# Kernel optimization log

Measured on AMD Instinct MI355X. Metric: run time of the kernel, lower is better.

The kernel has to match this reference:

```python
import jax, jax.numpy as jnp
import numpy as np
import math

B, S, D, H, F = 2, 2048, 1024, 16, 4096
DK = D // H
NEG_INF = -1000000000.0
EPS = 1e-5


def _layernorm(x, gamma, beta):
    # Faithful to source: torch.std default is unbiased (ddof=1), eps added to std
    mn = jnp.mean(x, axis=-1, keepdims=True)
    sd = jnp.std(x, axis=-1, keepdims=True, ddof=1)
    return (x - mn) / (sd + EPS) * gamma + beta


def _mha(xq, xkv, wq, bq, wk, bk, wv, bv, wo, bo, causal):
    b, sq, d = xq.shape
    sk = xkv.shape[1]
    q = (xq @ wq + bq).reshape(b, sq, H, DK).transpose(0, 2, 1, 3)   # [B,H,Sq,DK]
    k = (xkv @ wk + bk).reshape(b, sk, H, DK).transpose(0, 2, 1, 3)
    v = (xkv @ wv + bv).reshape(b, sk, H, DK).transpose(0, 2, 1, 3)
    scores = jnp.einsum('bhqd,bhkd->bhqk', q, k) / math.sqrt(DK)
    if causal:
        mask = jnp.triu(jnp.ones((sq, sk), dtype=scores.dtype), 1) * NEG_INF
        scores = scores + mask
    w = jax.nn.softmax(scores, axis=-1)
    att = jnp.einsum('bhqk,bhkd->bhqd', w, v).transpose(0, 2, 1, 3).reshape(b, sq, d)
    return att @ wo + bo


def setup_inputs() -> dict:
    key = jax.random.key(0)
    ks = jax.random.split(key, 32)
    it = iter(range(32))

    def lin(din, dout):
        kw = ks[next(it)]
        w = jax.random.normal(kw, (din, dout), jnp.float32) / math.sqrt(din)
        b = jnp.zeros((dout,), jnp.float32)
        return w, b

    X = jax.random.normal(ks[next(it)], (B, S, D), jnp.float32)
    y = jax.random.normal(ks[next(it)], (B, S, D), jnp.float32)
    wq1, bq1 = lin(D, D); wk1, bk1 = lin(D, D); wv1, bv1 = lin(D, D); wo1, bo1 = lin(D, D)
    wq2, bq2 = lin(D, D); wk2, bk2 = lin(D, D); wv2, bv2 = lin(D, D); wo2, bo2 = lin(D, D)
    wf1, bf1 = lin(D, F); wf2, bf2 = lin(F, D)
    g1 = jnp.ones((D,), jnp.float32); be1 = jnp.zeros((D,), jnp.float32)
    g2 = jnp.ones((D,), jnp.float32); be2 = jnp.zeros((D,), jnp.float32)
    g3 = jnp.ones((D,), jnp.float32); be3 = jnp.zeros((D,), jnp.float32)
    return dict(X=X, y=y,
                wq1=wq1, bq1=bq1, wk1=wk1, bk1=bk1, wv1=wv1, bv1=bv1, wo1=wo1, bo1=bo1,
                wq2=wq2, bq2=bq2, wk2=wk2, bk2=bk2, wv2=wv2, bv2=bv2, wo2=wo2, bo2=bo2,
                wf1=wf1, bf1=bf1, wf2=wf2, bf2=bf2,
                g1=g1, be1=be1, g2=g2, be2=be2, g3=g3, be3=be3)


def reference(X, y,
              wq1, bq1, wk1, bk1, wv1, bv1, wo1, bo1,
              wq2, bq2, wk2, bk2, wv2, bv2, wo2, bo2,
              wf1, bf1, wf2, bf2,
              g1, be1, g2, be2, g3, be3):
    # masked self-attention on decoder stream y (dropout = identity at inference)
    res = y
    out = _mha(y, y, wq1, bq1, wk1, bk1, wv1, bv1, wo1, bo1, causal=True)
    out = _layernorm(out + res, g1, be1)
    # cross-attention: queries from decoder, keys/values from encoder X
    res = out
    out = _mha(out, X, wq2, bq2, wk2, bk2, wv2, bv2, wo2, bo2, causal=False)
    out = _layernorm(out + res, g2, be2)
    # feed-forward (ReLU per intended semantics of the source)
    res = out
    out = jax.nn.relu(out @ wf1 + bf1) @ wf2 + bf2
    out = _layernorm(out + res, g3, be3)
    return out
```

## Files before the change

kernel.cpp:

```cpp
#include <hip/hip_runtime.h>

#define DEV __device__ __forceinline__

typedef __attribute__((ext_vector_type(8))) short short8;
typedef __attribute__((ext_vector_type(4))) float f32x4;
typedef __attribute__((ext_vector_type(4))) unsigned u32x4;

DEV unsigned short f2b(float f){
  unsigned r;
  asm("v_cvt_pk_bf16_f32 %0, %1, %1" : "=v"(r) : "v"(f));
  return (unsigned short)r;
}
DEV unsigned cvt_pk2(float lo, float hi){
  unsigned r;
  asm("v_cvt_pk_bf16_f32 %0, %1, %2" : "=v"(r) : "v"(lo), "v"(hi));
  return r;
}
DEV float b2f(unsigned short u){ unsigned v = ((unsigned)u)<<16; float f; __builtin_memcpy(&f,&v,4); return f; }

DEV void gload_lds16(const void* g, void* l){
  __builtin_amdgcn_global_load_lds((const __attribute__((address_space(1))) void*)g,
                                   (__attribute__((address_space(3))) void*)l, 16, 0, 0);
}

#define SCL 0.18033688011112042f

__global__ __launch_bounds__(256) void cvt_f32_bf16(
    const float* __restrict__ in, unsigned short* __restrict__ out, int n)
{
  int i = (blockIdx.x*256 + threadIdx.x)*4;
  if (i >= n) return;
  float4 v = *(const float4*)(in + i);
  uint2 o;
  o.x = cvt_pk2(v.x, v.y);
  o.y = cvt_pk2(v.z, v.w);
  *(uint2*)(out + i) = o;
}

struct TransAll {
  const float* W[10]; unsigned short* Wt[10];
  int K[10], N[10], swapxy[10];
};
__global__ __launch_bounds__(256) void transpose_cvt_all(TransAll p)
{
  const int z = blockIdx.z;
  const int bx = p.swapxy[z] ? blockIdx.y : blockIdx.x;
  const int by = p.swapxy[z] ? blockIdx.x : blockIdx.y;
  const int K = p.K[z], N = p.N[z];
  const int n0 = bx*32, k0 = by*32;
  if (n0 >= N || k0 >= K) return;
  const float* __restrict__ W = p.W[z];
  unsigned short* __restrict__ Wt = p.Wt[z];
  __shared__ float tile[32][33];
  int tx = threadIdx.x & 31, ty = threadIdx.x >> 5;
  #pragma unroll
  for (int j=0;j<32;j+=8)
    tile[ty+j][tx] = W[(size_t)(k0+ty+j)*N + n0+tx];
  __syncthreads();
  #pragma unroll
  for (int j=0;j<32;j+=8)
    Wt[(size_t)(n0+ty+j)*K + k0+tx] = f2b(tile[tx][ty+j]);
}

template<int EPI>
__global__ __launch_bounds__(256) void gemm_bt(
    const unsigned short* __restrict__ A,
    const unsigned short* __restrict__ Bt,
    const float* __restrict__ bias,
    unsigned short* __restrict__ C,
    int M, int N, int Kc, int LDA, int LDB)
{
  __shared__ alignas(16) unsigned short Asm_[128*64];
  __shared__ alignas(16) unsigned short Bsm_[128*64];
  const int tid = threadIdx.x;
  const int wave = tid>>6, lane = tid&63;
  const int r0 = lane&15, kq = (lane>>4)*8, cq = lane>>4;
  const int m0 = blockIdx.y*128, n0 = blockIdx.x*128;
  const int wr = wave>>1, wc = wave&1;
  const int koff = blockIdx.z * Kc;
  const bool addb = (blockIdx.z == 0);
  C += (size_t)blockIdx.z * M * N;
  const int swr = (r0&7)<<3;

  f32x4 zero4 = {0.f,0.f,0.f,0.f};
  f32x4 acc[4][4];
  #pragma unroll
  for (int m=0;m<4;m++)
    #pragma unroll
    for (int n=0;n<4;n++) acc[m][n]=zero4;

  const int nk = Kc>>6;
  for (int kt=0; kt<nk; kt++){
    #pragma unroll
    for (int i=0;i<4;i++){
      int idx = i*256 + tid;
      int row = idx>>3;
      int sc = ((idx&7) ^ (row&7))<<3;
      gload_lds16(A  + (size_t)(m0+row)*LDA + koff + (kt<<6) + sc, Asm_ + (size_t)idx*8);
      gload_lds16(Bt + (size_t)(n0+row)*LDB + koff + (kt<<6) + sc, Bsm_ + (size_t)idx*8);
    }
    __syncthreads();
    #pragma unroll
    for (int kk=0;kk<2;kk++){
      short8 a[4], b[4];
      #pragma unroll
      for (int m=0;m<4;m++)
        a[m] = *(const short8*)&Asm_[(((wr*64 + m*16 + r0)*64) + kk*32 + kq) ^ swr];
      #pragma unroll
      for (int n=0;n<4;n++)
        b[n] = *(const short8*)&Bsm_[(((wc*64 + n*16 + r0)*64) + kk*32 + kq) ^ swr];
      #pragma unroll
      for (int m=0;m<4;m++)
        #pragma unroll
        for (int n=0;n<4;n++)
          acc[m][n] = __builtin_amdgcn_mfma_f32_16x16x32_bf16(a[m], b[n], acc[m][n], 0,0,0);
    }
    __syncthreads();
  }

  #pragma unroll
  for (int n=0;n<4;n++){
    int col = n0 + wc*64 + n*16 + r0;
    float bs = addb ? bias[col] : 0.f;
    #pragma unroll
    for (int m=0;m<4;m++){
      int rowb = m0 + wr*64 + m*16 + cq*4;
      #pragma unroll
      for (int reg=0;reg<4;reg++){
        float v = acc[m][n][reg] + bs;
        if (EPI==1) v = fmaxf(v, 0.f);
        C[(size_t)(rowb+reg)*N + col] = f2b(v);
      }
    }
  }
}

struct QKVArgs { const unsigned short* Aw[3]; const float* bias[3]; unsigned short* out[3]; };
__global__ __launch_bounds__(256) void gemm_qkv(
    const unsigned short* __restrict__ Bt,
    QKVArgs args, int M, int K)
{
  __shared__ alignas(16) unsigned short Asm_[128*64];
  __shared__ alignas(16) unsigned short Bsm_[128*64];
  const int tid = threadIdx.x;
  const int wave = tid>>6, lane = tid&63;
  const int r0 = lane&15, kq = (lane>>4)*8, cq = lane>>4;
  const int m0 = blockIdx.y*128, n0 = blockIdx.x*128;
  const int wr = wave>>1, wc = wave&1;
  const int which = n0>>10;
  const unsigned short* __restrict__ A = args.Aw[which];
  const int swr = (r0&7)<<3;

  f32x4 zero4 = {0.f,0.f,0.f,0.f};
  f32x4 acc[4][4];
  #pragma unroll
  for (int m=0;m<4;m++)
    #pragma unroll
    for (int n=0;n<4;n++) acc[m][n]=zero4;

  const int nk = K>>6;
  for (int kt=0; kt<nk; kt++){
    #pragma unroll
    for (int i=0;i<4;i++){
      int idx = i*256 + tid;
      int row = idx>>3;
      int sc = ((idx&7) ^ (row&7))<<3;
      gload_lds16(A  + (size_t)(m0+row)*K + (kt<<6) + sc, Asm_ + (size_t)idx*8);
      gload_lds16(Bt + (size_t)(n0+row)*K + (kt<<6) + sc, Bsm_ + (size_t)idx*8);
    }
    __syncthreads();
    #pragma unroll
    for (int kk=0;kk<2;kk++){
      short8 a[4], b[4];
      #pragma unroll
      for (int m=0;m<4;m++)
        a[m] = *(const short8*)&Asm_[(((wr*64 + m*16 + r0)*64) + kk*32 + kq) ^ swr];
      #pragma unroll
      for (int n=0;n<4;n++)
        b[n] = *(const short8*)&Bsm_[(((wc*64 + n*16 + r0)*64) + kk*32 + kq) ^ swr];
      #pragma unroll
      for (int m=0;m<4;m++)
        #pragma unroll
        for (int n=0;n<4;n++)
          acc[m][n] = __builtin_amdgcn_mfma_f32_16x16x32_bf16(a[m], b[n], acc[m][n], 0,0,0);
    }
    __syncthreads();
  }

  const int n0l = n0 & 1023;
  unsigned short* __restrict__ Cout = args.out[which];
  const float* __restrict__ bp = args.bias[which];
  const bool isV = (which == 2);
  const float scl = (which == 0) ? SCL : 1.f;

  #pragma unroll
  for (int n=0;n<4;n++){
    int col = n0l + wc*64 + n*16 + r0;
    float bs = bp[col];
    int h_ = col>>6, dk = col&63;
    #pragma unroll
    for (int m=0;m<4;m++){
      int rowb = m0 + wr*64 + m*16 + cq*4;
      #pragma unroll
      for (int reg=0;reg<4;reg++){
        float v = (acc[m][n][reg] + bs) * scl;
        int row = rowb + reg;
        int b_ = row>>11, s_ = row&2047;
        if (isV){
          int sp = (s_ & ~31) | (((s_>>2)&3)<<3) | (((s_>>4)&1)<<2) | (s_&3);
          Cout[(((size_t)(b_*16+h_))*64 + dk)*2048 + sp] = f2b(v);
        } else {
          Cout[(((size_t)(b_*16+h_))*2048 + s_)*64 + dk] = f2b(v);
        }
      }
    }
  }
}

template<int MODE>
__global__ __launch_bounds__(256, 4) void attn_kernel(
    const unsigned short* __restrict__ Q,
    const unsigned short* __restrict__ K,
    const unsigned short* __restrict__ Vt,
    unsigned short* __restrict__ O,
    float* __restrict__ po, unsigned short* __restrict__ pob,
    float* __restrict__ ml)
{
  __shared__ alignas(16) unsigned short Ksm[2][64*64];
  __shared__ alignas(16) unsigned short Vsm[2][64*64];
  const int S = 2048, DK = 64;
  const int h = blockIdx.y, b = blockIdx.z;
  const int tid = threadIdx.x, wave = tid>>6, lane = tid&63;
  const int r0 = lane&15, kq = (lane>>4)*8, cq = lane>>4;

  int qb, t0, t1, chunk = 0;
  bool partial = false;
  if (MODE==1){
    int bx = blockIdx.x;
    if (bx < 32){ qb = bx; t0 = 0; t1 = (qb<15?qb:15); chunk = 0; partial = (qb>=16); }
    else        { qb = bx-16; t0 = 16; t1 = qb; chunk = 1; partial = true; }
  } else {
    int bx = blockIdx.x;
    if (bx < 32){ qb = bx; t0 = 0; t1 = 15; chunk = 0; }
    else        { qb = bx-32; t0 = 16; t1 = 31; chunk = 1; }
    partial = true;
  }

  const unsigned short* qh = Q  + ((size_t)(b*16+h))*S*DK;
  const unsigned short* kh = K  + ((size_t)(b*16+h))*S*DK;
  const unsigned short* vh = Vt + ((size_t)(b*16+h))*DK*S;

  const int idx0 = tid, idx1 = 256 + tid;
  const int row0 = idx0>>3, row1 = idx1>>3;
  const int cb0 = ((idx0&7) ^ (row0&7))<<3;
  const int cb1 = ((idx1&7) ^ (row1&7))<<3;
  const unsigned short* kg0 = kh + (size_t)row0*64 + cb0;
  const unsigned short* kg1 = kh + (size_t)row1*64 + cb1;
  const unsigned short* vg0 = vh + (size_t)row0*2048 + cb0;
  const unsigned short* vg1 = vh + (size_t)row1*2048 + cb1;
  const int l0 = wave*512, l1 = 2048 + wave*512;
  const int swr = (r0&7)<<3;

  short8 qa[2];
  {
    int qrow = qb*64 + wave*16 + r0;
    qa[0] = *(const short8*)&qh[(size_t)qrow*DK + kq];
    qa[1] = *(const short8*)&qh[(size_t)qrow*DK + 32 + kq];
  }
  short8 vones;
  #pragma unroll
  for (int j=0;j<8;j++) vones[j] = (short)0x3F80;

  f32x4 zero4 = {0.f,0.f,0.f,0.f};
  f32x4 o[4];
  float lr = 0.f;
  #pragma unroll
  for (int n=0;n<4;n++) o[n]=zero4;

  gload_lds16(kg0 + (size_t)t0*4096, &Ksm[0][l0]);
  gload_lds16(kg1 + (size_t)t0*4096, &Ksm[0][l1]);
  gload_lds16(vg0 + (size_t)t0*64,   &Vsm[0][l0]);
  gload_lds16(vg1 + (size_t)t0*64,   &Vsm[0][l1]);

  int cur = 0;
  for (int t=t0; t<=t1; t++){
    if (t < t1){
      gload_lds16(kg0 + (size_t)(t+1)*4096, &Ksm[cur^1][l0]);
      gload_lds16(kg1 + (size_t)(t+1)*4096, &Ksm[cur^1][l1]);
      gload_lds16(vg0 + (size_t)(t+1)*64,   &Vsm[cur^1][l0]);
      gload_lds16(vg1 + (size_t)(t+1)*64,   &Vsm[cur^1][l1]);
      asm volatile("s_waitcnt vmcnt(4)" ::: "memory");
    } else {
      asm volatile("s_waitcnt vmcnt(0)" ::: "memory");
    }
    __builtin_amdgcn_s_barrier();
    asm volatile("" ::: "memory");

    f32x4 sv[4];
    #pragma unroll
    for (int n=0;n<4;n++) sv[n]=zero4;
    #pragma unroll
    for (int n=0;n<4;n++)
      #pragma unroll
      for (int kk=0;kk<2;kk++){
        short8 kb = *(const short8*)&Ksm[cur][(((n*16 + r0)*64) + kk*32 + kq) ^ swr];
        sv[n] = __builtin_amdgcn_mfma_f32_16x16x32_bf16(kb, qa[kk], sv[n], 0,0,0);
      }
    if (MODE==1 && t==qb){
      const int qg = wave*16 + r0;
      #pragma unroll
      for (int n=0;n<4;n++)
        #pragma unroll
        for (int reg=0;reg<4;reg++){
          if (n*16 + cq*4 + reg > qg) sv[n][reg] += -1000000000.0f;
        }
    }

    #pragma unroll
    for (int n=0;n<4;n++)
      #pragma unroll
      for (int reg=0;reg<4;reg++)
        sv[n][reg] = exp2f(sv[n][reg]);

    short8 pa[2];
    #pragma unroll
    for (int kk=0;kk<2;kk++){
      u32x4 w;
      w[0] = cvt_pk2(sv[2*kk][0],   sv[2*kk][1]);
      w[1] = cvt_pk2(sv[2*kk][2],   sv[2*kk][3]);
      w[2] = cvt_pk2(sv[2*kk+1][0], sv[2*kk+1][1]);
      w[3] = cvt_pk2(sv[2*kk+1][2], sv[2*kk+1][3]);
      pa[kk] = __builtin_bit_cast(short8, w);
    }

    {
      f32x4 ls = zero4;
      ls = __builtin_amdgcn_mfma_f32_16x16x32_bf16(vones, pa[0], ls, 0,0,0);
      ls = __builtin_amdgcn_mfma_f32_16x16x32_bf16(vones, pa[1], ls, 0,0,0);
      lr += ls[0];
    }

    #pragma unroll
    for (int n=0;n<4;n++)
      #pragma unroll
      for (int kk=0;kk<2;kk++){
        short8 vb = *(const short8*)&Vsm[cur][(((n*16 + r0)*64) + kk*32 + cq*8) ^ swr];
        o[n] = __builtin_amdgcn_mfma_f32_16x16x32_bf16(vb, pa[kk], o[n], 0,0,0);
      }

    asm volatile("" ::: "memory");
    __builtin_amdgcn_s_barrier();
    asm volatile("" ::: "memory");
    cur ^= 1;
  }

  if (MODE==1 && partial){
    float* pop = po + (size_t)chunk*2097152;
    float* mlp = ml + (size_t)chunk*32768;
    const int bh = b*16 + h, qb16 = qb - 16;
    const int rowIdx = (bh*16 + qb16)*64 + wave*16 + r0;
    if (cq == 0) mlp[rowIdx] = lr;
    #pragma unroll
    for (int n=0;n<4;n++){
      float4 v; v.x=o[n][0]; v.y=o[n][1]; v.z=o[n][2]; v.w=o[n][3];
      *(float4*)&pop[(size_t)rowIdx*64 + n*16 + cq*4] = v;
    }
  } else if (MODE==2){
    unsigned short* pop = pob + (size_t)chunk*4194304;
    float* mlp = ml + (size_t)chunk*65536;
    const int bh = b*16 + h;
    const int rowIdx = (bh*32 + qb)*64 + wave*16 + r0;
    if (cq == 0) mlp[rowIdx] = lr;
    #pragma unroll
    for (int n=0;n<4;n++){
      uint2 w;
      w.x = cvt_pk2(o[n][0], o[n][1]);
      w.y = cvt_pk2(o[n][2], o[n][3]);
      *(uint2*)(pop + (size_t)rowIdx*64 + n*16 + cq*4) = w;
    }
  } else {
    const int sg = qb*64 + wave*16 + r0;
    const float inv = 1.f / lr;
    unsigned short* op = O + ((size_t)b*S + sg)*1024 + h*64;
    #pragma unroll
    for (int n=0;n<4;n++){
      uint2 w;
      w.x = cvt_pk2(o[n][0]*inv, o[n][1]*inv);
      w.y = cvt_pk2(o[n][2]*inv, o[n][3]*inv);
      *(uint2*)(op + n*16 + cq*4) = w;
    }
  }
}

__global__ __launch_bounds__(256) void attn_merge(
    const float* __restrict__ po, const float* __restrict__ ml,
    unsigned short* __restrict__ O)
{
  int gid = blockIdx.x*256 + threadIdx.x;
  int row = gid>>4, dq = (gid&15)*4;
  float l0 = ml[row], l1 = ml[32768 + row];
  float inv = 1.f / (l0 + l1);
  float4 v0 = *(const float4*)(po + (size_t)row*64 + dq);
  float4 v1 = *(const float4*)(po + 2097152 + (size_t)row*64 + dq);
  float r0 = (v0.x + v1.x)*inv;
  float r1 = (v0.y + v1.y)*inv;
  float r2 = (v0.z + v1.z)*inv;
  float r3 = (v0.w + v1.w)*inv;
  int bh = row>>10, qb16 = (row>>6)&15, qr = row&63;
  int b = bh>>4, h = bh&15;
  int s = (16+qb16)*64 + qr;
  unsigned short* op = O + ((size_t)b*2048 + s)*1024 + h*64 + dq;
  uint2 out; out.x = cvt_pk2(r0, r1); out.y = cvt_pk2(r2, r3);
  *(uint2*)op = out;
}

__global__ __launch_bounds__(256) void attn_merge_x(
    const unsigned short* __restrict__ pob, const float* __restrict__ ml,
    unsigned short* __restrict__ O)
{
  int gid = blockIdx.x*256 + threadIdx.x;
  int row = gid>>4, dq = (gid&15)*4;
  float l0 = ml[row], l1 = ml[65536 + row];
  float inv = 1.f / (l0 + l1);
  ushort4 u0 = *(const ushort4*)(pob + (size_t)row*64 + dq);
  ushort4 u1 = *(const ushort4*)(pob + 4194304 + (size_t)row*64 + dq);
  float r0 = (b2f(u0.x) + b2f(u1.x))*inv;
  float r1 = (b2f(u0.y) + b2f(u1.y))*inv;
  float r2 = (b2f(u0.z) + b2f(u1.z))*inv;
  float r3 = (b2f(u0.w) + b2f(u1.w))*inv;
  int bh = row>>11, s = row&2047;
  int b = bh>>4, h = bh&15;
  unsigned short* op = O + ((size_t)b*2048 + s)*1024 + h*64 + dq;
  uint2 out; out.x = cvt_pk2(r0, r1); out.y = cvt_pk2(r2, r3);
  *(uint2*)op = out;
}

template<int OUT_F32>
__global__ __launch_bounds__(256) void add_ln3(
    const unsigned short* __restrict__ a0, const unsigned short* __restrict__ a1,
    const unsigned short* __restrict__ r,
    const float* __restrict__ g, const float* __restrict__ be, void* outp)
{
  const int row = blockIdx.x, tid = threadIdx.x;
  const size_t base = (size_t)row*1024 + tid*4;
  ushort4 va = *(const ushort4*)(a0 + base);
  ushort4 vb_ = *(const ushort4*)(a1 + base);
  ushort4 vr = *(const ushort4*)(r + base);
  float x[4];
  x[0] = b2f(va.x)+b2f(vb_.x)+b2f(vr.x);
  x[1] = b2f(va.y)+b2f(vb_.y)+b2f(vr.y);
  x[2] = b2f(va.z)+b2f(vb_.z)+b2f(vr.z);
  x[3] = b2f(va.w)+b2f(vb_.w)+b2f(vr.w);
  float s = x[0]+x[1]+x[2]+x[3];
  float ss = x[0]*x[0]+x[1]*x[1]+x[2]*x[2]+x[3]*x[3];
  #pragma unroll
  for (int d=1;d<64;d<<=1){ s += __shfl_xor(s,d,64); ss += __shfl_xor(ss,d,64); }
  __shared__ float rs[4], rss[4];
  int wave = tid>>6, lane = tid&63;
  if (lane==0){ rs[wave]=s; rss[wave]=ss; }
  __syncthreads();
  s = rs[0]+rs[1]+rs[2]+rs[3];
  ss = rss[0]+rss[1]+rss[2]+rss[3];
  float mean = s*(1.f/1024.f);
  float var = (ss - 1024.f*mean*mean)*(1.f/1023.f);
  float sd = sqrtf(fmaxf(var,0.f));
  float inv = 1.f/(sd + 1e-5f);
  float4 vg = *(const float4*)(g + tid*4);
  float4 vbe = *(const float4*)(be + tid*4);
  float o0 = (x[0]-mean)*inv*vg.x+vbe.x;
  float o1 = (x[1]-mean)*inv*vg.y+vbe.y;
  float o2 = (x[2]-mean)*inv*vg.z+vbe.z;
  float o3 = (x[3]-mean)*inv*vg.w+vbe.w;
  if (OUT_F32){
    float4 vo; vo.x=o0; vo.y=o1; vo.z=o2; vo.w=o3;
    *(float4*)((float*)outp + base) = vo;
  } else {
    uint2 vo; vo.x = cvt_pk2(o0,o1); vo.y = cvt_pk2(o2,o3);
    *(uint2*)((unsigned short*)outp + base) = vo;
  }
}

extern "C" void kernel_launch(void* const* d_in, const int* in_sizes, int n_in,
                              void* d_out, int out_size, void* d_ws, size_t ws_size,
                              hipStream_t stream)
{
  typedef const float* cf;
  cf X   = (cf)d_in[0],  y   = (cf)d_in[1];
  cf wq1 = (cf)d_in[2],  bq1 = (cf)d_in[3],  wk1 = (cf)d_in[4],  bk1 = (cf)d_in[5];
  cf wv1 = (cf)d_in[6],  bv1 = (cf)d_in[7],  wo1 = (cf)d_in[8],  bo1 = (cf)d_in[9];
  cf wq2 = (cf)d_in[10], bq2 = (cf)d_in[11], wk2 = (cf)d_in[12], bk2 = (cf)d_in[13];
  cf wv2 = (cf)d_in[14], bv2 = (cf)d_in[15], wo2 = (cf)d_in[16], bo2 = (cf)d_in[17];
  cf wf1 = (cf)d_in[18], bf1 = (cf)d_in[19], wf2 = (cf)d_in[20], bf2 = (cf)d_in[21];
  cf g1  = (cf)d_in[22], be1 = (cf)d_in[23], g2  = (cf)d_in[24], be2 = (cf)d_in[25];
  cf g3  = (cf)d_in[26], be3 = (cf)d_in[27];

  char* ws = (char*)d_ws;
  const size_t MB = 1u<<20;
  unsigned short* wq1t = (unsigned short*)(ws + 0*MB);
  unsigned short* wk1t = (unsigned short*)(ws + 2*MB);
  unsigned short* wv1t = (unsigned short*)(ws + 4*MB);
  unsigned short* wo1t = (unsigned short*)(ws + 6*MB);
  unsigned short* wq2t = (unsigned short*)(ws + 8*MB);
  unsigned short* wk2t = (unsigned short*)(ws + 10*MB);
  unsigned short* wv2t = (unsigned short*)(ws + 12*MB);
  unsigned short* wo2t = (unsigned short*)(ws + 14*MB);
  unsigned short* wf1t = (unsigned short*)(ws + 16*MB);
  unsigned short* wf2t = (unsigned short*)(ws + 24*MB);
  unsigned short* Qb   = (unsigned short*)(ws + 32*MB);
  unsigned short* Kb   = (unsigned short*)(ws + 40*MB);
  unsigned short* Vtb  = (unsigned short*)(ws + 48*MB);
  unsigned short* attno= (unsigned short*)(ws + 56*MB);
  unsigned short* hbuf = (unsigned short*)(ws + 32*MB);
  unsigned short* part = (unsigned short*)(ws + 64*MB);
  float*          poF  = (float*)(ws + 64*MB);
  unsigned short* pobF = (unsigned short*)(ws + 64*MB);
  float*          mlF  = (float*)(ws + 80*MB);
  unsigned short* x1b  = (unsigned short*)(ws + 80*MB);
  unsigned short* slot = (unsigned short*)(ws + 88*MB);
  unsigned short* yb = slot, *Xb = slot, *x2b = slot;
  float*          mlX  = (float*)(ws + 88*MB);

  dim3 blk(256);
  const int NTOK = 2*2048*1024;
  cvt_f32_bf16<<<NTOK/1024, blk, 0, stream>>>(y, yb, NTOK);

  {
    TransAll tp;
    const float* Ws[10]   = {wq1,wk1,wv1,wo1,wq2,wk2,wv2,wo2,wf1,wf2};
    unsigned short* Ts[10]= {wq1t,wk1t,wv1t,wo1t,wq2t,wk2t,wv2t,wo2t,wf1t,wf2t};
    for (int i=0;i<10;i++){
      tp.W[i]=Ws[i]; tp.Wt[i]=Ts[i];
      tp.K[i] = (i==9)?4096:1024;
      tp.N[i] = (i==8)?4096:1024;
      tp.swapxy[i] = (i==9)?1:0;
    }
    transpose_cvt_all<<<dim3(128,32,10), blk, 0, stream>>>(tp);
  }

  dim3 gqkv(24,32);
  dim3 gs(8,32,2);
  dim3 gff1(32,32,1);
  dim3 gac(48,16,2);
  dim3 gax(64,16,2);

  {
    QKVArgs a1;
    a1.Aw[0]=yb; a1.Aw[1]=yb; a1.Aw[2]=yb;
    a1.bias[0]=bq1; a1.bias[1]=bk1; a1.bias[2]=bv1;
    a1.out[0]=Qb; a1.out[1]=Kb; a1.out[2]=Vtb;
    gemm_qkv<<<gqkv, blk, 0, stream>>>(wq1t, a1, 4096, 1024);
  }
  attn_kernel<1><<<gac, blk, 0, stream>>>(Qb, Kb, Vtb, attno, poF, nullptr, mlF);
  attn_merge<<<2048, blk, 0, stream>>>(poF, mlF, attno);
  gemm_bt<0><<<gs, blk, 0, stream>>>(attno, wo1t, bo1, part, 4096, 1024, 512, 1024, 1024);
  add_ln3<0><<<4096, blk, 0, stream>>>(part, part+4194304, yb, g1, be1, x1b);

  cvt_f32_bf16<<<NTOK/1024, blk, 0, stream>>>(X, Xb, NTOK);
  {
    QKVArgs a2;
    a2.Aw[0]=x1b; a2.Aw[1]=Xb; a2.Aw[2]=Xb;
    a2.bias[0]=bq2; a2.bias[1]=bk2; a2.bias[2]=bv2;
    a2.out[0]=Qb; a2.out[1]=Kb; a2.out[2]=Vtb;
    gemm_qkv<<<gqkv, blk, 0, stream>>>(wq2t, a2, 4096, 1024);
  }
  attn_kernel<2><<<gax, blk, 0, stream>>>(Qb, Kb, Vtb, attno, nullptr, pobF, mlX);
  attn_merge_x<<<4096, blk, 0, stream>>>(pobF, mlX, attno);
  gemm_bt<0><<<gs, blk, 0, stream>>>(attno, wo2t, bo2, part, 4096, 1024, 512, 1024, 1024);
  add_ln3<0><<<4096, blk, 0, stream>>>(part, part+4194304, x1b, g2, be2, x2b);

  gemm_bt<1><<<gff1, blk, 0, stream>>>(x2b, wf1t, bf1, hbuf, 4096, 4096, 1024, 1024, 1024);
  gemm_bt<0><<<gs, blk, 0, stream>>>(hbuf, wf2t, bf2, part, 4096, 1024, 2048, 4096, 4096);
  add_ln3<1><<<4096, blk, 0, stream>>>(part, part+4194304, x2b, g3, be3, d_out);
}
```

Baseline: 385.4 us.

## Process two query tiles per block in cross-attention to reuse K/V tiles

Splits the templated attention kernel into a causal kernel and a dedicated cross-attention kernel. Each cross-attention block now handles 128 query rows, two 64-row sub-tiles per wave, against the same LDS-staged K/V tiles, so K/V global loads and barriers are shared across twice the queries. The grid is halved to match, and launch bounds drop to 2 blocks per CU because register use roughly doubles. The trade-off is lower occupancy and fewer blocks to hide latency, in exchange for less K/V traffic per query row.

```diff
diff --git a/kernel.cpp b/kernel.cpp
--- a/kernel.cpp
+++ b/kernel.cpp
@@ -217,14 +217,12 @@
   }
 }
 
-template<int MODE>
-__global__ __launch_bounds__(256, 4) void attn_kernel(
+__global__ __launch_bounds__(256, 4) void attn_causal(
     const unsigned short* __restrict__ Q,
     const unsigned short* __restrict__ K,
     const unsigned short* __restrict__ Vt,
     unsigned short* __restrict__ O,
-    float* __restrict__ po, unsigned short* __restrict__ pob,
-    float* __restrict__ ml)
+    float* __restrict__ po, float* __restrict__ ml)
 {
   __shared__ alignas(16) unsigned short Ksm[2][64*64];
   __shared__ alignas(16) unsigned short Vsm[2][64*64];
@@ -235,15 +233,10 @@
 
   int qb, t0, t1, chunk = 0;
   bool partial = false;
-  if (MODE==1){
+  {
     int bx = blockIdx.x;
     if (bx < 32){ qb = bx; t0 = 0; t1 = (qb<15?qb:15); chunk = 0; partial = (qb>=16); }
     else        { qb = bx-16; t0 = 16; t1 = qb; chunk = 1; partial = true; }
-  } else {
-    int bx = blockIdx.x;
-    if (bx < 32){ qb = bx; t0 = 0; t1 = 15; chunk = 0; }
-    else        { qb = bx-32; t0 = 16; t1 = 31; chunk = 1; }
-    partial = true;
   }
 
   const unsigned short* qh = Q  + ((size_t)(b*16+h))*S*DK;
@@ -258,7 +251,7 @@
   const unsigned short* kg1 = kh + (size_t)row1*64 + cb1;
   const unsigned short* vg0 = vh + (size_t)row0*2048 + cb0;
   const unsigned short* vg1 = vh + (size_t)row1*2048 + cb1;
-  const int l0 = wave*512, l1 = 2048 + wave*512;
+  const int ld0 = wave*512, ld1 = 2048 + wave*512;
   const int swr = (r0&7)<<3;
 
   short8 qa[2];
@@ -277,18 +270,18 @@
   #pragma unroll
   for (int n=0;n<4;n++) o[n]=zero4;
 
-  gload_lds16(kg0 + (size_t)t0*4096, &Ksm[0][l0]);
-  gload_lds16(kg1 + (size_t)t0*4096, &Ksm[0][l1]);
-  gload_lds16(vg0 + (size_t)t0*64,   &Vsm[0][l0]);
-  gload_lds16(vg1 + (size_t)t0*64,   &Vsm[0][l1]);
+  gload_lds16(kg0 + (size_t)t0*4096, &Ksm[0][ld0]);
+  gload_lds16(kg1 + (size_t)t0*4096, &Ksm[0][ld1]);
+  gload_lds16(vg0 + (size_t)t0*64,   &Vsm[0][ld0]);
+  gload_lds16(vg1 + (size_t)t0*64,   &Vsm[0][ld1]);
 
   int cur = 0;
   for (int t=t0; t<=t1; t++){
     if (t < t1){
-      gload_lds16(kg0 + (size_t)(t+1)*4096, &Ksm[cur^1][l0]);
-      gload_lds16(kg1 + (size_t)(t+1)*4096, &Ksm[cur^1][l1]);
-      gload_lds16(vg0 + (size_t)(t+1)*64,   &Vsm[cur^1][l0]);
-      gload_lds16(vg1 + (size_t)(t+1)*64,   &Vsm[cur^1][l1]);
+      gload_lds16(kg0 + (size_t)(t+1)*4096, &Ksm[cur^1][ld0]);
+      gload_lds16(kg1 + (size_t)(t+1)*4096, &Ksm[cur^1][ld1]);
+      gload_lds16(vg0 + (size_t)(t+1)*64,   &Vsm[cur^1][ld0]);
+      gload_lds16(vg1 + (size_t)(t+1)*64,   &Vsm[cur^1][ld1]);
       asm volatile("s_waitcnt vmcnt(4)" ::: "memory");
     } else {
       asm volatile("s_waitcnt vmcnt(0)" ::: "memory");
@@ -306,7 +299,7 @@
         short8 kb = *(const short8*)&Ksm[cur][(((n*16 + r0)*64) + kk*32 + kq) ^ swr];
         sv[n] = __builtin_amdgcn_mfma_f32_16x16x32_bf16(kb, qa[kk], sv[n], 0,0,0);
       }
-    if (MODE==1 && t==qb){
+    if (t==qb){
       const int qg = wave*16 + r0;
       #pragma unroll
       for (int n=0;n<4;n++)
@@ -354,7 +347,7 @@
     cur ^= 1;
   }
 
-  if (MODE==1 && partial){
+  if (partial){
     float* pop = po + (size_t)chunk*2097152;
     float* mlp = ml + (size_t)chunk*32768;
     const int bh = b*16 + h, qb16 = qb - 16;
@@ -365,19 +358,6 @@
       float4 v; v.x=o[n][0]; v.y=o[n][1]; v.z=o[n][2]; v.w=o[n][3];
       *(float4*)&pop[(size_t)rowIdx*64 + n*16 + cq*4] = v;
     }
-  } else if (MODE==2){
-    unsigned short* pop = pob + (size_t)chunk*4194304;
-    float* mlp = ml + (size_t)chunk*65536;
-    const int bh = b*16 + h;
-    const int rowIdx = (bh*32 + qb)*64 + wave*16 + r0;
-    if (cq == 0) mlp[rowIdx] = lr;
-    #pragma unroll
-    for (int n=0;n<4;n++){
-      uint2 w;
-      w.x = cvt_pk2(o[n][0], o[n][1]);
-      w.y = cvt_pk2(o[n][2], o[n][3]);
-      *(uint2*)(pop + (size_t)rowIdx*64 + n*16 + cq*4) = w;
-    }
   } else {
     const int sg = qb*64 + wave*16 + r0;
     const float inv = 1.f / lr;
@@ -389,6 +369,160 @@
       w.y = cvt_pk2(o[n][2]*inv, o[n][3]*inv);
       *(uint2*)(op + n*16 + cq*4) = w;
     }
+  }
+}
+
+__global__ __launch_bounds__(256, 2) void attn_cross2(
+    const unsigned short* __restrict__ Q,
+    const unsigned short* __restrict__ K,
+    const unsigned short* __restrict__ Vt,
+    unsigned short* __restrict__ pob,
+    float* __restrict__ ml)
+{
+  __shared__ alignas(16) unsigned short Ksm[2][64*64];
+  __shared__ alignas(16) unsigned short Vsm[2][64*64];
+  const int S = 2048, DK = 64;
+  const int h = blockIdx.y, b = blockIdx.z;
+  const int tid = threadIdx.x, wave = tid>>6, lane = tid&63;
+  const int r0 = lane&15, kq = (lane>>4)*8, cq = lane>>4;
+
+  int qB, t0, t1, chunk;
+  {
+    int bx = blockIdx.x;
+    if (bx < 16){ qB = bx; t0 = 0; t1 = 15; chunk = 0; }
+    else        { qB = bx-16; t0 = 16; t1 = 31; chunk = 1; }
+  }
+
+  const unsigned short* qh = Q  + ((size_t)(b*16+h))*S*DK;
+  const unsigned short* kh = K  + ((size_t)(b*16+h))*S*DK;
+  const unsigned short* vh = Vt + ((size_t)(b*16+h))*DK*S;
+
+  const int idx0 = tid, idx1 = 256 + tid;
+  const int row0 = idx0>>3, row1 = idx1>>3;
+  const int cb0 = ((idx0&7) ^ (row0&7))<<3;
+  const int cb1 = ((idx1&7) ^ (row1&7))<<3;
+  const unsigned short* kg0 = kh + (size_t)row0*64 + cb0;
+  const unsigned short* kg1 = kh + (size_t)row1*64 + cb1;
+  const unsigned short* vg0 = vh + (size_t)row0*2048 + cb0;
+  const unsigned short* vg1 = vh + (size_t)row1*2048 + cb1;
+  const int ld0 = wave*512, ld1 = 2048 + wave*512;
+  const int swr = (r0&7)<<3;
+
+  short8 qa0[2], qa1[2];
+  {
+    int qrow = qB*128 + wave*16 + r0;
+    qa0[0] = *(const short8*)&qh[(size_t)qrow*DK + kq];
+    qa0[1] = *(const short8*)&qh[(size_t)qrow*DK + 32 + kq];
+    qa1[0] = *(const short8*)&qh[(size_t)(qrow+64)*DK + kq];
+    qa1[1] = *(const short8*)&qh[(size_t)(qrow+64)*DK + 32 + kq];
+  }
+  short8 vones;
+  #pragma unroll
+  for (int j=0;j<8;j++) vones[j] = (short)0x3F80;
+
+  f32x4 zero4 = {0.f,0.f,0.f,0.f};
+  f32x4 o0[4], o1[4];
+  float lr0 = 0.f, lr1 = 0.f;
+  #pragma unroll
+  for (int n=0;n<4;n++){ o0[n]=zero4; o1[n]=zero4; }
+
+  gload_lds16(kg0 + (size_t)t0*4096, &Ksm[0][ld0]);
+  gload_lds16(kg1 + (size_t)t0*4096, &Ksm[0][ld1]);
+  gload_lds16(vg0 + (size_t)t0*64,   &Vsm[0][ld0]);
+  gload_lds16(vg1 + (size_t)t0*64,   &Vsm[0][ld1]);
+
+  int cur = 0;
+  for (int t=t0; t<=t1; t++){
+    if (t < t1){
+      gload_lds16(kg0 + (size_t)(t+1)*4096, &Ksm[cur^1][ld0]);
+      gload_lds16(kg1 + (size_t)(t+1)*4096, &Ksm[cur^1][ld1]);
+      gload_lds16(vg0 + (size_t)(t+1)*64,   &Vsm[cur^1][ld0]);
+      gload_lds16(vg1 + (size_t)(t+1)*64,   &Vsm[cur^1][ld1]);
+      asm volatile("s_waitcnt vmcnt(4)" ::: "memory");
+    } else {
+      asm volatile("s_waitcnt vmcnt(0)" ::: "memory");
+    }
+    __builtin_amdgcn_s_barrier();
+    asm volatile("" ::: "memory");
+
+    f32x4 sa[4], sb[4];
+    #pragma unroll
+    for (int n=0;n<4;n++){ sa[n]=zero4; sb[n]=zero4; }
+    #pragma unroll
+    for (int n=0;n<4;n++)
+      #pragma unroll
+      for (int kk=0;kk<2;kk++){
+        short8 kb = *(const short8*)&Ksm[cur][(((n*16 + r0)*64) + kk*32 + kq) ^ swr];
+        sa[n] = __builtin_amdgcn_mfma_f32_16x16x32_bf16(kb, qa0[kk], sa[n], 0,0,0);
+        sb[n] = __builtin_amdgcn_mfma_f32_16x16x32_bf16(kb, qa1[kk], sb[n], 0,0,0);
+      }
+
+    #pragma unroll
+    for (int n=0;n<4;n++)
+      #pragma unroll
+      for (int reg=0;reg<4;reg++){
+        sa[n][reg] = exp2f(sa[n][reg]);
+        sb[n][reg] = exp2f(sb[n][reg]);
+      }
+
+    short8 pa0[2], pa1[2];
+    #pragma unroll
+    for (int kk=0;kk<2;kk++){
+      u32x4 w0, w1;
+      w0[0] = cvt_pk2(sa[2*kk][0],   sa[2*kk][1]);
+      w0[1] = cvt_pk2(sa[2*kk][2],   sa[2*kk][3]);
+      w0[2] = cvt_pk2(sa[2*kk+1][0], sa[2*kk+1][1]);
+      w0[3] = cvt_pk2(sa[2*kk+1][2], sa[2*kk+1][3]);
+      pa0[kk] = __builtin_bit_cast(short8, w0);
+      w1[0] = cvt_pk2(sb[2*kk][0],   sb[2*kk][1]);
+      w1[1] = cvt_pk2(sb[2*kk][2],   sb[2*kk][3]);
+      w1[2] = cvt_pk2(sb[2*kk+1][0], sb[2*kk+1][1]);
+      w1[3] = cvt_pk2(sb[2*kk+1][2], sb[2*kk+1][3]);
+      pa1[kk] = __builtin_bit_cast(short8, w1);
+    }
+
+    {
+      f32x4 ls = zero4;
+      ls = __builtin_amdgcn_mfma_f32_16x16x32_bf16(vones, pa0[0], ls, 0,0,0);
+      ls = __builtin_amdgcn_mfma_f32_16x16x32_bf16(vones, pa0[1], ls, 0,0,0);
+      lr0 += ls[0];
+      f32x4 ls2 = zero4;
+      ls2 = __builtin_amdgcn_mfma_f32_16x16x32_bf16(vones, pa1[0], ls2, 0,0,0);
+      ls2 = __builtin_amdgcn_mfma_f32_16x16x32_bf16(vones, pa1[1], ls2, 0,0,0);
+      lr1 += ls2[0];
+    }
+
+    #pragma unroll
+    for (int n=0;n<4;n++)
+      #pragma unroll
+      for (int kk=0;kk<2;kk++){
+        short8 vb = *(const short8*)&Vsm[cur][(((n*16 + r0)*64) + kk*32 + cq*8) ^ swr];
+        o0[n] = __builtin_amdgcn_mfma_f32_16x16x32_bf16(vb, pa0[kk], o0[n], 0,0,0);
+        o1[n] = __builtin_amdgcn_mfma_f32_16x16x32_bf16(vb, pa1[kk], o1[n], 0,0,0);
+      }
+
+    asm volatile("" ::: "memory");
+    __builtin_amdgcn_s_barrier();
+    asm volatile("" ::: "memory");
+    cur ^= 1;
+  }
+
+  unsigned short* pop = pob + (size_t)chunk*4194304;
+  float* mlp = ml + (size_t)chunk*65536;
+  const int bh = b*16 + h;
+  const int rowA = (bh*16 + qB)*128 + wave*16 + r0;
+  const int rowB = rowA + 64;
+  if (cq == 0){ mlp[rowA] = lr0; mlp[rowB] = lr1; }
+  #pragma unroll
+  for (int n=0;n<4;n++){
+    uint2 w0;
+    w0.x = cvt_pk2(o0[n][0], o0[n][1]);
+    w0.y = cvt_pk2(o0[n][2], o0[n][3]);
+    *(uint2*)(pop + (size_t)rowA*64 + n*16 + cq*4) = w0;
+    uint2 w1;
+    w1.x = cvt_pk2(o1[n][0], o1[n][1]);
+    w1.y = cvt_pk2(o1[n][2], o1[n][3]);
+    *(uint2*)(pop + (size_t)rowB*64 + n*16 + cq*4) = w1;
   }
 }
 
@@ -541,7 +675,7 @@
   dim3 gs(8,32,2);
   dim3 gff1(32,32,1);
   dim3 gac(48,16,2);
-  dim3 gax(64,16,2);
+  dim3 gax(32,16,2);
 
   {
     QKVArgs a1;
@@ -550,7 +684,7 @@
     a1.out[0]=Qb; a1.out[1]=Kb; a1.out[2]=Vtb;
     gemm_qkv<<<gqkv, blk, 0, stream>>>(wq1t, a1, 4096, 1024);
   }
-  attn_kernel<1><<<gac, blk, 0, stream>>>(Qb, Kb, Vtb, attno, poF, nullptr, mlF);
+  attn_causal<<<gac, blk, 0, stream>>>(Qb, Kb, Vtb, attno, poF, mlF);
   attn_merge<<<2048, blk, 0, stream>>>(poF, mlF, attno);
   gemm_bt<0><<<gs, blk, 0, stream>>>(attno, wo1t, bo1, part, 4096, 1024, 512, 1024, 1024);
   add_ln3<0><<<4096, blk, 0, stream>>>(part, part+4194304, yb, g1, be1, x1b);
@@ -563,7 +697,7 @@
     a2.out[0]=Qb; a2.out[1]=Kb; a2.out[2]=Vtb;
     gemm_qkv<<<gqkv, blk, 0, stream>>>(wq2t, a2, 4096, 1024);
   }
-  attn_kernel<2><<<gax, blk, 0, stream>>>(Qb, Kb, Vtb, attno, nullptr, pobF, mlX);
+  attn_cross2<<<gax, blk, 0, stream>>>(Qb, Kb, Vtb, pobF, mlX);
   attn_merge_x<<<4096, blk, 0, stream>>>(pobF, mlX, attno);
   gemm_bt<0><<<gs, blk, 0, stream>>>(attno, wo2t, bo2, part, 4096, 1024, 512, 1024, 1024);
   add_ln3<0><<<4096, blk, 0, stream>>>(part, part+4194304, x1b, g2, be2, x2b);
```

Result: no change. 381.2 us (median of 3 runs) (-1.1%).
